# Kernel optimization log

Hardware: AMD Instinct MI355X
Metric: run time of the kernel (lower is better)

The kernel has to match this reference:

```python
import jax, jax.numpy as jnp
import numpy as np

N = 50000
E = 200000
H = 8          # heads
C = 256        # out channels per head
IN = 256       # in_dim
NEG_SLOPE = 0.2
EPS = 1e-16    # PyG softmax denominator epsilon


def setup_inputs() -> dict:
    key = jax.random.key(0)
    k1, k2, k3, k4, k5, k6 = jax.random.split(key, 6)
    glorot = lambda k, shape, fan: jax.random.normal(k, shape, jnp.float32) * np.sqrt(2.0 / fan)
    x = jax.random.normal(k1, (N, IN), jnp.float32)
    edge_index = jax.random.randint(k2, (2, E), 0, N, jnp.int32)
    W = glorot(k3, (IN, H * C), IN + H * C)          # lin_src weight (shared src/dst)
    att_src = glorot(k4, (H, C), C)
    att_dst = glorot(k5, (H, C), C)
    bias = jnp.zeros((C,), jnp.float32)              # concat=False -> bias size out_dim
    return {"x": x, "edge_index": edge_index, "W": W,
            "att_src": att_src, "att_dst": att_dst, "bias": bias}


def reference(x, edge_index, W, att_src, att_dst, bias):
    # Linear projection -> per-head features [N, H, C]
    h = (x @ W).reshape(N, H, C)
    # Per-node attention logits [N, H]
    a_src = jnp.einsum('nhc,hc->nh', h, att_src)
    a_dst = jnp.einsum('nhc,hc->nh', h, att_dst)
    src, dst = edge_index[0], edge_index[1]
    # Edge scores with leaky relu [E, H]
    e = jax.nn.leaky_relu(a_src[src] + a_dst[dst], NEG_SLOPE)
    # Segment softmax over incoming edges of each dst node
    m = jax.ops.segment_max(e, dst, num_segments=N)          # [N, H]
    e = jnp.exp(e - m[dst])
    denom = jax.ops.segment_sum(e, dst, num_segments=N)      # [N, H]
    alpha = e / (denom[dst] + EPS)                           # [E, H]
    # Weighted scatter-add aggregation [N, H, C]
    msg = h[src] * alpha[:, :, None]
    out = jax.ops.segment_sum(msg, dst, num_segments=N)
    # concat=False -> mean over heads, then bias
    return out.mean(axis=1) + bias
```

## Files before the change

kernel.cpp:

```cpp
#include <hip/hip_runtime.h>
#include <hip/hip_bf16.h>

#define NN 50000
#define EE 200000
#define HH 8
#define CC 256
#define IND 256
#define HC 2048
#define NEG 0.2f
#define EPSV 1e-16f

typedef __attribute__((ext_vector_type(8))) short short8;
typedef __attribute__((ext_vector_type(4))) float f32x4;

__device__ __forceinline__ float b2f(unsigned short u) {
  return __uint_as_float(((unsigned)u) << 16);
}
__device__ __forceinline__ unsigned short f2b(float f) {
  unsigned u = __float_as_uint(f);
  unsigned r = (u + 0x7FFFu + ((u >> 16) & 1u)) >> 16;
  return (unsigned short)r;
}

__global__ __launch_bounds__(1024) void k_wt2(const float* __restrict__ W,
                                              unsigned short* __restrict__ wt2) {
  __shared__ float tile[32][33];
  int kk0 = blockIdx.x * 32;
  int c0 = blockIdx.y * 32;
  int tx = threadIdx.x & 31, ty = threadIdx.x >> 5;
  int h = kk0 >> 8;
  int k = (kk0 & 255) + ty;
  tile[ty][tx] = W[(size_t)k * HC + h * 256 + c0 + tx] * 0.125f;
  __syncthreads();
  wt2[(size_t)(c0 + ty) * HC + kk0 + tx] = f2b(tile[tx][ty]);
}

__global__ __launch_bounds__(256) void k_wfold(const float* __restrict__ W,
                                               const float* __restrict__ att_s,
                                               const float* __restrict__ att_d,
                                               float* __restrict__ wsrc,
                                               float* __restrict__ wdst) {
  int in = blockIdx.x;
  int t = threadIdx.x;
  int h = t >> 5;
  int c0 = (t & 31) * 8;
  float ps = 0.f, pd = 0.f;
#pragma unroll
  for (int j = 0; j < 8; ++j) {
    float wv = W[(size_t)in * HC + h * 256 + c0 + j];
    ps += wv * att_s[h * 256 + c0 + j];
    pd += wv * att_d[h * 256 + c0 + j];
  }
#pragma unroll
  for (int o = 16; o >= 1; o >>= 1) {
    ps += __shfl_down(ps, o, 32);
    pd += __shfl_down(pd, o, 32);
  }
  if ((t & 31) == 0) {
    wsrc[in * HH + h] = ps;
    wdst[in * HH + h] = pd;
  }
}

__global__ __launch_bounds__(256) void k_alog2c(const float* __restrict__ x,
                                                const float* __restrict__ wsrc,
                                                const float* __restrict__ wdst,
                                                const int* __restrict__ dstn,
                                                unsigned short* __restrict__ xb,
                                                float* __restrict__ a_src,
                                                float* __restrict__ a_dst,
                                                int* __restrict__ deg) {
  int gid = blockIdx.x * 256 + threadIdx.x;
  if (gid < EE) atomicAdd(&deg[dstn[gid]], 1);

  const int l = threadIdx.x & 63;
  const int gwave = (blockIdx.x * 256 + threadIdx.x) >> 6;
  const int nwaves = (gridDim.x * 256) >> 6;
  float ws_[4][8], wd_[4][8];
#pragma unroll
  for (int j = 0; j < 4; ++j) {
#pragma unroll
    for (int h = 0; h < 8; ++h) {
      ws_[j][h] = wsrc[(l * 4 + j) * HH + h];
      wd_[j][h] = wdst[(l * 4 + j) * HH + h];
    }
  }
  for (int n = gwave; n < NN; n += nwaves) {
    float4 xv = *(const float4*)(x + (size_t)n * IND + l * 4);
    float xa[4] = {xv.x, xv.y, xv.z, xv.w};
    ushort4 o = make_ushort4(f2b(xv.x), f2b(xv.y), f2b(xv.z), f2b(xv.w));
    *(ushort4*)(xb + (size_t)n * IND + l * 4) = o;
    float as[8] = {}, ad[8] = {};
#pragma unroll
    for (int j = 0; j < 4; ++j)
#pragma unroll
      for (int h = 0; h < 8; ++h) {
        as[h] += xa[j] * ws_[j][h];
        ad[h] += xa[j] * wd_[j][h];
      }
#pragma unroll
    for (int o2 = 32; o2 >= 1; o2 >>= 1) {
#pragma unroll
      for (int h = 0; h < 8; ++h) {
        as[h] += __shfl_down(as[h], o2);
        ad[h] += __shfl_down(ad[h], o2);
      }
    }
    if (l == 0) {
#pragma unroll
      for (int h = 0; h < 8; ++h) {
        a_src[n * HH + h] = as[h];
        a_dst[n * HH + h] = ad[h];
      }
    }
  }
}

__global__ __launch_bounds__(1024) void k_scanA(const int* __restrict__ deg,
                                                int* __restrict__ incl, int* __restrict__ bsum) {
  __shared__ int s[1024];
  int tid = threadIdx.x;
  int i = blockIdx.x * 1024 + tid;
  s[tid] = (i < NN) ? deg[i] : 0;
  __syncthreads();
  for (int o = 1; o < 1024; o <<= 1) {
    int add = (tid >= o) ? s[tid - o] : 0;
    __syncthreads();
    s[tid] += add;
    __syncthreads();
  }
  if (i < NN) incl[i] = s[tid];
  if (tid == 1023) bsum[blockIdx.x] = s[1023];
}

__global__ void k_scanB(int* bsum, int nb) {
  int l = threadIdx.x & 63;
  int v = (l < nb) ? bsum[l] : 0;
  int incl = v;
#pragma unroll
  for (int o = 1; o < 64; o <<= 1) {
    int t = __shfl_up(incl, o, 64);
    if (l >= o) incl += t;
  }
  if (l < nb) bsum[l] = incl - v;
}

__global__ __launch_bounds__(1024) void k_scanC(const int* __restrict__ deg, const int* __restrict__ incl,
                                                const int* __restrict__ bsum, int* __restrict__ row_start,
                                                int* __restrict__ cursor) {
  int i = blockIdx.x * 1024 + threadIdx.x;
  if (i < NN) {
    int ex = bsum[i >> 10] + incl[i] - deg[i];
    row_start[i] = ex;
    cursor[i] = ex;
  }
  if (i == 0) row_start[NN] = EE;
}

__global__ void k_scatter(const int* __restrict__ srcn, const int* __restrict__ dstn,
                          int* __restrict__ cursor, int* __restrict__ csr_src) {
  int e = blockIdx.x * 256 + threadIdx.x;
  if (e < EE) {
    int d = dstn[e];
    int p = atomicAdd(&cursor[d], 1);
    csr_src[p] = srcn[e];
  }
}

__global__ __launch_bounds__(256) void k_aggxf(const unsigned short* __restrict__ xb,
                                               const float* __restrict__ a_src,
                                               const float* __restrict__ a_dst,
                                               const int* __restrict__ row_start,
                                               const int* __restrict__ csr_src,
                                               unsigned short* __restrict__ y) {
  __shared__ float w_s[4][8][8];
  __shared__ float inv_s[4][8];
  const int l = threadIdx.x & 63;
  const int wv = threadIdx.x >> 6;
  const int n = blockIdx.x * 4 + wv;
  if (n >= NN) return;
  const int start = row_start[n];
  const int D = row_start[n + 1] - start;
  unsigned short* yp = y + (size_t)n * HC + l * 4;
  if (D == 0) {
    ushort4 z = make_ushort4(0, 0, 0, 0);
#pragma unroll
    for (int h = 0; h < 8; ++h) *(ushort4*)(yp + h * 256) = z;
    return;
  }
  const int h = l & 7;
  const int e8 = l >> 3;
  const float adst = a_dst[n * HH + h];

  float ssum = 0.f;
  float acc[8][4] = {};
  for (int base = 0; base < D; base += 8) {
    int nch = min(8, D - base);
    int e = base + e8;
    int s = 0;
    float we = 0.f;
    if (e < D) {
      s = csr_src[start + e];
      float xv = a_src[s * HH + h] + adst;
      float lg = (xv > 0.f) ? xv : NEG * xv;
      we = __expf(fminf(lg, 60.f));
      ssum += we;
    }
    w_s[wv][e8][h] = we;
    for (int ee = 0; ee < nch; ++ee) {
      int se = __shfl(s, ee * 8, 64);
      f32x4 a0 = *(const f32x4*)&w_s[wv][ee][0];
      f32x4 a1 = *(const f32x4*)&w_s[wv][ee][4];
      ushort4 v = *(const ushort4*)(xb + (size_t)se * IND + l * 4);
      float x0 = b2f(v.x), x1 = b2f(v.y), x2 = b2f(v.z), x3 = b2f(v.w);
#pragma unroll
      for (int hh = 0; hh < 8; ++hh) {
        float a = (hh < 4) ? a0[hh] : a1[hh - 4];
        acc[hh][0] += a * x0;
        acc[hh][1] += a * x1;
        acc[hh][2] += a * x2;
        acc[hh][3] += a * x3;
      }
    }
  }
#pragma unroll
  for (int mask = 8; mask < 64; mask <<= 1) ssum += __shfl_xor(ssum, mask, 64);
  if (e8 == 0) inv_s[wv][h] = 1.f / (ssum + EPSV);
  f32x4 i0 = *(const f32x4*)&inv_s[wv][0];
  f32x4 i1 = *(const f32x4*)&inv_s[wv][4];
#pragma unroll
  for (int hh = 0; hh < 8; ++hh) {
    float iv = (hh < 4) ? i0[hh] : i1[hh - 4];
    ushort4 o = make_ushort4(f2b(acc[hh][0] * iv), f2b(acc[hh][1] * iv),
                             f2b(acc[hh][2] * iv), f2b(acc[hh][3] * iv));
    *(ushort4*)(yp + hh * 256) = o;
  }
}

__global__ __launch_bounds__(512) void k_gemm2(const unsigned short* __restrict__ y,
                                               const unsigned short* __restrict__ wt2,
                                               const float* __restrict__ bias,
                                               float* __restrict__ out) {
  __shared__ unsigned short As[128 * 64];
  __shared__ unsigned short Bs[256 * 64];
  const int t = threadIdx.x;
  const int lane = t & 63;
  const int w = t >> 6;
  const int wr = w >> 2;
  const int wc = w & 3;
  const int l16 = lane & 15;
  const int lq = lane >> 4;
  const int m0 = blockIdx.x * 128;

  f32x4 acc[4][4] = {};

  const int so = t * 16;

  for (int ks = 0; ks < 32; ++ks) {
    const int k0 = ks * 64;
#pragma unroll
    for (int i = 0; i < 2; ++i) {
      int o = i * 8192 + so;
      int row = o >> 7;
      int cg = ((o >> 4) & 7) ^ (row & 7);
      const unsigned short* srcA = y + (size_t)(m0 + row) * HC + k0 + cg * 8;
      __builtin_amdgcn_global_load_lds(
          (const __attribute__((address_space(1))) void*)srcA,
          (__attribute__((address_space(3))) void*)((char*)As + o), 16, 0, 0);
    }
#pragma unroll
    for (int i = 0; i < 4; ++i) {
      int o = i * 8192 + so;
      int row = o >> 7;
      int cg = ((o >> 4) & 7) ^ (row & 7);
      const unsigned short* srcB = wt2 + (size_t)row * HC + k0 + cg * 8;
      __builtin_amdgcn_global_load_lds(
          (const __attribute__((address_space(1))) void*)srcB,
          (__attribute__((address_space(3))) void*)((char*)Bs + o), 16, 0, 0);
    }
    __syncthreads();
#pragma unroll
    for (int kk = 0; kk < 2; ++kk) {
      short8 af[4], bf[4];
#pragma unroll
      for (int m = 0; m < 4; ++m) {
        int row = wr * 64 + m * 16 + l16;
        int byte = row * 128 + (((kk * 4 + lq) ^ (row & 7)) << 4);
        af[m] = *(const short8*)((const char*)As + byte);
      }
#pragma unroll
      for (int n = 0; n < 4; ++n) {
        int row = wc * 64 + n * 16 + l16;
        int byte = row * 128 + (((kk * 4 + lq) ^ (row & 7)) << 4);
        bf[n] = *(const short8*)((const char*)Bs + byte);
      }
      __builtin_amdgcn_s_setprio(1);
#pragma unroll
      for (int m = 0; m < 4; ++m)
#pragma unroll
        for (int n = 0; n < 4; ++n)
          acc[m][n] = __builtin_amdgcn_mfma_f32_16x16x32_bf16(af[m], bf[n], acc[m][n], 0, 0, 0);
      __builtin_amdgcn_s_setprio(0);
    }
    __syncthreads();
  }

  const int r0 = lq * 4;
#pragma unroll
  for (int n = 0; n < 4; ++n) {
    int gcol = wc * 64 + n * 16 + l16;
    float bv = bias[gcol];
#pragma unroll
    for (int m = 0; m < 4; ++m) {
#pragma unroll
      for (int r = 0; r < 4; ++r) {
        int grow = m0 + wr * 64 + m * 16 + r0 + r;
        if (grow < NN) out[(size_t)grow * CC + gcol] = acc[m][n][r] + bv;
      }
    }
  }
}

extern "C" void kernel_launch(void* const* d_in, const int* in_sizes, int n_in,
                              void* d_out, int out_size, void* d_ws, size_t ws_size,
                              hipStream_t stream) {
  (void)in_sizes; (void)n_in; (void)out_size; (void)ws_size;
  const float* x = (const float*)d_in[0];
  const int* ei = (const int*)d_in[1];
  const float* W = (const float*)d_in[2];
  const float* att_s = (const float*)d_in[3];
  const float* att_d = (const float*)d_in[4];
  const float* bias = (const float*)d_in[5];
  float* out = (float*)d_out;
  const int* srcp = ei;
  const int* dstp = ei + EE;

  char* ws = (char*)d_ws;
  size_t off = 0;
  auto alloc = [&](size_t bytes) {
    void* p = ws + off;
    off = (off + bytes + 255) & ~(size_t)255;
    return p;
  };
  unsigned short* y = (unsigned short*)alloc((size_t)NN * HC * 2);
  unsigned short* xb = (unsigned short*)alloc((size_t)NN * IND * 2);
  unsigned short* wt2 = (unsigned short*)alloc((size_t)HC * IND * 2);
  float* wsrc = (float*)alloc((size_t)IND * HH * 4);
  float* wdst = (float*)alloc((size_t)IND * HH * 4);
  float* a_src = (float*)alloc((size_t)NN * HH * 4);
  float* a_dst = (float*)alloc((size_t)NN * HH * 4);
  int* deg = (int*)alloc((size_t)NN * 4);
  int* incl = (int*)alloc((size_t)NN * 4);
  int* row_start = (int*)alloc((size_t)(NN + 1) * 4);
  int* cursor = (int*)alloc((size_t)NN * 4);
  int* csr_src = (int*)alloc((size_t)EE * 4);
  int* bsum = (int*)alloc(256);

  hipMemsetAsync(deg, 0, (size_t)NN * 4, stream);

  k_wt2<<<dim3(HC / 32, CC / 32), 1024, 0, stream>>>(W, wt2);
  k_wfold<<<IND, 256, 0, stream>>>(W, att_s, att_d, wsrc, wdst);
  k_alog2c<<<832, 256, 0, stream>>>(x, wsrc, wdst, dstp, xb, a_src, a_dst, deg);
  int nb = (NN + 1023) / 1024;
  k_scanA<<<nb, 1024, 0, stream>>>(deg, incl, bsum);
  k_scanB<<<1, 64, 0, stream>>>(bsum, nb);
  k_scanC<<<nb, 1024, 0, stream>>>(deg, incl, bsum, row_start, cursor);
  k_scatter<<<(EE + 255) / 256, 256, 0, stream>>>(srcp, dstp, cursor, csr_src);
  k_aggxf<<<(NN + 3) / 4, 256, 0, stream>>>(xb, a_src, a_dst, row_start, csr_src, y);
  k_gemm2<<<(NN + 127) / 128, 512, 0, stream>>>(y, wt2, bias, out);
}
```

Before: 242.7 us.

## Split-K the final GEMM across two blocks and fold scanB into scanC

The final GEMM (K=2048) is split into two K halves via a second grid dimension, with partial results combined through float atomicAdd into a zeroed output. Bias is added only by the first half. This doubles the block count from 391 to 782 so more CUs are busy, at the cost of an extra memset of the output and atomic read-modify-write traffic. Separately, the block-sum scan kernel is removed by having each scanC block recompute the 49-entry prefix itself, saving one launch.

```diff
diff --git a/kernel.cpp b/kernel.cpp
--- a/kernel.cpp
+++ b/kernel.cpp
@@ -133,24 +133,26 @@
   if (tid == 1023) bsum[blockIdx.x] = s[1023];
 }
 
-__global__ void k_scanB(int* bsum, int nb) {
-  int l = threadIdx.x & 63;
-  int v = (l < nb) ? bsum[l] : 0;
-  int incl = v;
-#pragma unroll
-  for (int o = 1; o < 64; o <<= 1) {
-    int t = __shfl_up(incl, o, 64);
-    if (l >= o) incl += t;
-  }
-  if (l < nb) bsum[l] = incl - v;
-}
-
 __global__ __launch_bounds__(1024) void k_scanC(const int* __restrict__ deg, const int* __restrict__ incl,
                                                 const int* __restrict__ bsum, int* __restrict__ row_start,
                                                 int* __restrict__ cursor) {
-  int i = blockIdx.x * 1024 + threadIdx.x;
+  __shared__ int base_s;
+  int tid = threadIdx.x;
+  if (tid < 64) {
+    int nb = gridDim.x;
+    int v = (tid < nb) ? bsum[tid] : 0;
+    int p = v;
+#pragma unroll
+    for (int o = 1; o < 64; o <<= 1) {
+      int tt = __shfl_up(p, o, 64);
+      if (tid >= o) p += tt;
+    }
+    if (tid == (int)blockIdx.x) base_s = p - v;
+  }
+  __syncthreads();
+  int i = blockIdx.x * 1024 + tid;
   if (i < NN) {
-    int ex = bsum[i >> 10] + incl[i] - deg[i];
+    int ex = base_s + incl[i] - deg[i];
     row_start[i] = ex;
     cursor[i] = ex;
   }
@@ -251,13 +253,14 @@
   const int l16 = lane & 15;
   const int lq = lane >> 4;
   const int m0 = blockIdx.x * 128;
+  const int kbase = blockIdx.y * 1024;
 
   f32x4 acc[4][4] = {};
 
   const int so = t * 16;
 
-  for (int ks = 0; ks < 32; ++ks) {
-    const int k0 = ks * 64;
+  for (int ks = 0; ks < 16; ++ks) {
+    const int k0 = kbase + ks * 64;
 #pragma unroll
     for (int i = 0; i < 2; ++i) {
       int o = i * 8192 + so;
@@ -309,13 +312,13 @@
 #pragma unroll
   for (int n = 0; n < 4; ++n) {
     int gcol = wc * 64 + n * 16 + l16;
-    float bv = bias[gcol];
+    float bv = (blockIdx.y == 0) ? bias[gcol] : 0.f;
 #pragma unroll
     for (int m = 0; m < 4; ++m) {
 #pragma unroll
       for (int r = 0; r < 4; ++r) {
         int grow = m0 + wr * 64 + m * 16 + r0 + r;
-        if (grow < NN) out[(size_t)grow * CC + gcol] = acc[m][n][r] + bv;
+        if (grow < NN) atomicAdd(&out[(size_t)grow * CC + gcol], acc[m][n][r] + bv);
       }
     }
   }
@@ -357,15 +360,15 @@
   int* bsum = (int*)alloc(256);
 
   hipMemsetAsync(deg, 0, (size_t)NN * 4, stream);
+  hipMemsetAsync(out, 0, (size_t)NN * CC * 4, stream);
 
   k_wt2<<<dim3(HC / 32, CC / 32), 1024, 0, stream>>>(W, wt2);
   k_wfold<<<IND, 256, 0, stream>>>(W, att_s, att_d, wsrc, wdst);
   k_alog2c<<<832, 256, 0, stream>>>(x, wsrc, wdst, dstp, xb, a_src, a_dst, deg);
   int nb = (NN + 1023) / 1024;
   k_scanA<<<nb, 1024, 0, stream>>>(deg, incl, bsum);
-  k_scanB<<<1, 64, 0, stream>>>(bsum, nb);
   k_scanC<<<nb, 1024, 0, stream>>>(deg, incl, bsum, row_start, cursor);
   k_scatter<<<(EE + 255) / 256, 256, 0, stream>>>(srcp, dstp, cursor, csr_src);
   k_aggxf<<<(NN + 3) / 4, 256, 0, stream>>>(xb, a_src, a_dst, row_start, csr_src, y);
-  k_gemm2<<<(NN + 127) / 128, 512, 0, stream>>>(y, wt2, bias, out);
-}
+  k_gemm2<<<dim3((NN + 127) / 128, 2), 512, 0, stream>>>(y, wt2, bias, out);
+}
```

Result: slower. 320.4 us (+32.0%).
